# Performance work log

Hardware: AMD Instinct MI355X
Metric: run time of the kernel (lower is better)

The kernel has to match this reference:

```python
import jax, jax.numpy as jnp
import numpy as np

B, S, D = 2, 2048, 2048
H, G = 32, 8            # n_head, n_kv_groups
DH = D // H             # 64
HG = H // G             # heads per group = 4


def setup_inputs() -> dict:
    key = jax.random.key(0)
    ks = jax.random.split(key, 7)
    kv_dim = G * DH
    return {
        "q": jax.random.normal(ks[0], (B, S, D), jnp.float32),
        "k": jax.random.normal(ks[1], (B, S, D), jnp.float32),
        "v": jax.random.normal(ks[2], (B, S, D), jnp.float32),
        "mask": jnp.tril(jnp.ones((S, S), jnp.bool_)),  # causal
        "w_q": jax.random.normal(ks[3], (D, D), jnp.float32) * 0.02,
        "w_k": jax.random.normal(ks[4], (kv_dim, D), jnp.float32) * 0.02,
        "w_v": jax.random.normal(ks[5], (kv_dim, D), jnp.float32) * 0.02,
        "w_out": jax.random.normal(ks[6], (D, D), jnp.float32) * 0.02,
    }


def reference(q, k, v, mask, w_q, w_k, w_v, w_out):
    scale = 1.0 / np.sqrt(DH).astype(np.float32)
    # projections (F.linear: x @ W.T)
    qp = (q @ w_q.T).reshape(B, S, G, HG, DH)   # [b s g h d]
    kp = (k @ w_k.T).reshape(B, S, G, DH)       # [b t g d]
    vp = (v @ w_v.T).reshape(B, S, G, DH)
    # grouped attention scores [b g h s t]
    scores = jnp.einsum('bsghd,btgd->bghst', qp, kp) * scale
    scores = jnp.where(mask[None, None, None], scores, jnp.float32(-jnp.inf))
    attn = jax.nn.softmax(scores, axis=-1)
    out = jnp.einsum('bghst,btgd->bsghd', attn, vp).reshape(B, S, D)
    return out @ w_out.T
```

## Files before the change

kernel.cpp:

```cpp
#include <hip/hip_runtime.h>
#include <hip/hip_bf16.h>
#include <stdint.h>

#define B_SZ 2
#define S_LEN 2048
#define D_MODEL 2048
#define NH 32
#define NG 8
#define HGRP 4
#define DHEAD 64
#define KV_DIM 512
#define M_TOK 4096
#define KVB 64
#define QBLK 256
#define N_ITEMS2 768

typedef __attribute__((ext_vector_type(8))) short bf16x8;
typedef __attribute__((ext_vector_type(4))) float f32x4;
typedef __attribute__((ext_vector_type(16))) float f32x16;

__device__ inline unsigned short f2bf(float x) {
    uint32_t u = __builtin_bit_cast(uint32_t, x);
    uint32_t r = (u + 0x7fffu + ((u >> 16) & 1u)) >> 16;
    return (unsigned short)r;
}

__device__ inline uint32_t cvtpk(float lo, float hi) {
    uint32_t r;
    asm("v_cvt_pk_bf16_f32 %0, %1, %2" : "=v"(r) : "v"(lo), "v"(hi));
    return r;
}

__device__ inline void plswap(uint32_t& a, uint32_t& b) {
    asm volatile("v_permlane32_swap_b32 %0, %1" : "+v"(a), "+v"(b));
}

__device__ inline float bf2f(unsigned short u) {
    uint32_t x = ((uint32_t)u) << 16;
    return __builtin_bit_cast(float, x);
}

__device__ inline void async_copy16(const void* g, void* l) {
    __builtin_amdgcn_global_load_lds(
        (const __attribute__((address_space(1))) void*)g,
        (__attribute__((address_space(3))) void*)l,
        16, 0, 0);
}

__device__ inline void gbar() {
    asm volatile("" ::: "memory");
    __builtin_amdgcn_s_barrier();
    asm volatile("" ::: "memory");
}
__device__ inline void lgkm0() {
    asm volatile("s_waitcnt lgkmcnt(0)" ::: "memory");
    __builtin_amdgcn_sched_barrier(0);
}

__global__ __launch_bounds__(256) void cvt_all(const float* __restrict__ q,
                                               const float* __restrict__ k,
                                               const float* __restrict__ v,
                                               const float* __restrict__ wq,
                                               const float* __restrict__ wk,
                                               const float* __restrict__ wv,
                                               const float* __restrict__ wo,
                                               unsigned short* __restrict__ qb,
                                               unsigned short* __restrict__ kb,
                                               unsigned short* __restrict__ vb,
                                               unsigned short* __restrict__ wqb,
                                               unsigned short* __restrict__ wkvb,
                                               unsigned short* __restrict__ wob,
                                               unsigned int* __restrict__ cnt) {
    const int i = blockIdx.x * 256 + threadIdx.x;
    if (i == 0) *cnt = 0u;
    const float* src; unsigned short* dst; int j;
    if (i < 1048576)      { src = q;  dst = qb;  j = i; }
    else if (i < 2097152) { src = k;  dst = kb;  j = i - 1048576; }
    else if (i < 3145728) { src = v;  dst = vb;  j = i - 2097152; }
    else if (i < 3670016) { src = wq; dst = wqb; j = i - 3145728; }
    else if (i < 3801088) { src = wk; dst = wkvb; j = i - 3670016; }
    else if (i < 3932160) { src = wv; dst = wkvb + (size_t)KV_DIM * D_MODEL; j = i - 3801088; }
    else                  { src = wo; dst = wob; j = i - 3932160; }
    const float4* p = reinterpret_cast<const float4*>(src) + (size_t)j * 2;
    float4 a = p[0], b = p[1];
    union { unsigned short u[8]; uint4 v4; } r;
    r.u[0] = f2bf(a.x); r.u[1] = f2bf(a.y); r.u[2] = f2bf(a.z); r.u[3] = f2bf(a.w);
    r.u[4] = f2bf(b.x); r.u[5] = f2bf(b.y); r.u[6] = f2bf(b.z); r.u[7] = f2bf(b.w);
    reinterpret_cast<uint4*>(dst)[j] = r.v4;
}

#define SCALE_Q 0.1803368867f
#define GK 2048

template<int WHICH>
__global__ __launch_bounds__(512, 2) void gemm8(const unsigned short* __restrict__ Aq,
                                                const unsigned short* __restrict__ Ak,
                                                const unsigned short* __restrict__ Av,
                                                const unsigned short* __restrict__ Bq,
                                                const unsigned short* __restrict__ Bkv,
                                                unsigned short* __restrict__ out_q,
                                                unsigned short* __restrict__ out_k,
                                                unsigned short* __restrict__ out_v,
                                                float* __restrict__ out_f) {
    __shared__ __align__(16) char lds[131072];

    const int tid = threadIdx.x;
    const int lane = tid & 63;
    const int w = tid >> 6;
    const int wm = w >> 2, wn = w & 3;
    const int l15 = lane & 15, l4 = lane >> 4;

    const int nblk = (WHICH == 0) ? 192 : 128;
    int bid = blockIdx.x;
    bid = (bid & 7) * (nblk >> 3) + (bid >> 3);
    const int mb = bid & 15, nb = bid >> 4;
    const int m0 = mb * 256;

    const unsigned short* Ap;
    const unsigned short* Bp;
    int mode = 0, n0q = 0;
    if (WHICH == 1) {
        Ap = Aq; Bp = Bq + (size_t)(nb * 256) * GK; n0q = nb * 256;
    } else if (nb < 8) {
        Ap = Aq; Bp = Bq + (size_t)(nb * 256) * GK; mode = 0; n0q = nb * 256;
    } else if (nb < 10) {
        Ap = Ak; Bp = Bkv + (size_t)((nb - 8) * 256) * GK; mode = 1; n0q = (nb - 8) * 256;
    } else {
        Ap = Av; Bp = Bkv + (size_t)((nb - 10) * 256 + 512) * GK; mode = 2; n0q = (nb - 10) * 256;
    }

    const int srow = tid >> 3;
    const int gcol = (((tid & 7) * 16) ^ ((srow & 7) << 4)) >> 1;
    char* const myl = lds + tid * 16;

    auto stageA = [&](int tile, int half) {
        char* dst = myl + (tile & 1) * 32768 + half * 16384;
        const unsigned short* src = Ap + (size_t)(m0 + half * 128 + srow) * GK + tile * 64 + gcol;
        async_copy16(src, dst);
        async_copy16(src + (size_t)64 * GK, dst + 8192);
    };
    auto stageB = [&](int tile, int half) {
        char* dst = myl + 65536 + (tile & 1) * 32768 + half * 16384;
        const unsigned short* src = Bp + (size_t)(half * 128 + srow) * GK + tile * 64 + gcol;
        async_copy16(src, dst);
        async_copy16(src + (size_t)64 * GK, dst + 8192);
    };

    bf16x8 af[4][2], bf[4][2];
    auto loadA = [&](int buf, int mhalf) {
        const char* base = lds + buf * 32768;
#pragma unroll
        for (int mi = 0; mi < 4; ++mi) {
            const int r = wm * 128 + mhalf * 64 + mi * 16 + l15;
#pragma unroll
            for (int ks = 0; ks < 2; ++ks)
                af[mi][ks] = *reinterpret_cast<const bf16x8*>(
                    base + r * 128 + ((ks * 64 + l4 * 16) ^ ((r & 7) << 4)));
        }
    };
    auto loadB = [&](int buf, int nhalf) {
        const char* base = lds + 65536 + buf * 32768;
#pragma unroll
        for (int ni2 = 0; ni2 < 2; ++ni2) {
            const int ni = nhalf * 2 + ni2;
            const int r = wn * 64 + ni * 16 + l15;
#pragma unroll
            for (int ks = 0; ks < 2; ++ks)
                bf[ni][ks] = *reinterpret_cast<const bf16x8*>(
                    base + r * 128 + ((ks * 64 + l4 * 16) ^ ((r & 7) << 4)));
        }
    };

    f32x4 acc[8][4] = {};
    auto mfma16 = [&](int mq, int nq) {
        __builtin_amdgcn_s_setprio(1);
#pragma unroll
        for (int mi = 0; mi < 4; ++mi)
#pragma unroll
            for (int ni2 = 0; ni2 < 2; ++ni2)
#pragma unroll
                for (int ks = 0; ks < 2; ++ks)
                    acc[mq * 4 + mi][nq * 2 + ni2] = __builtin_amdgcn_mfma_f32_16x16x32_bf16(
                        af[mi][ks], bf[nq * 2 + ni2][ks], acc[mq * 4 + mi][nq * 2 + ni2], 0, 0, 0);
        __builtin_amdgcn_s_setprio(0);
    };

    stageA(0, 0); stageA(0, 1); stageB(0, 0); stageB(0, 1); stageB(1, 0); stageB(1, 1);
    asm volatile("s_waitcnt vmcnt(4)" ::: "memory");
    gbar();

    for (int i = 0; i < 16; ++i) {
        const int u = 2 * i;
        const bool nl = (i < 15);
        loadA(0, 0); loadB(0, 0); stageA(u + 1, 0);
        gbar(); lgkm0(); mfma16(0, 0); gbar();
        loadB(0, 1); stageA(u + 1, 1);
        gbar(); lgkm0(); mfma16(0, 1); gbar();
        loadA(0, 1); if (nl) stageB(u + 2, 0);
        gbar(); lgkm0(); mfma16(1, 0); gbar();
        if (nl) stageB(u + 2, 1);
        gbar(); mfma16(1, 1);
        if (nl) asm volatile("s_waitcnt vmcnt(4)" ::: "memory");
        else    asm volatile("s_waitcnt vmcnt(0)" ::: "memory");
        gbar();
        loadA(1, 0); loadB(1, 0); if (nl) stageA(u + 2, 0);
        gbar(); lgkm0(); mfma16(0, 0); gbar();
        loadB(1, 1); if (nl) stageA(u + 2, 1);
        gbar(); lgkm0(); mfma16(0, 1); gbar();
        loadA(1, 1); if (nl) stageB(u + 3, 0);
        gbar(); lgkm0(); mfma16(1, 0); gbar();
        if (nl) stageB(u + 3, 1);
        gbar(); mfma16(1, 1);
        if (nl) asm volatile("s_waitcnt vmcnt(4)" ::: "memory");
        gbar();
    }

    if (WHICH == 1) {
#pragma unroll
        for (int mi = 0; mi < 8; ++mi) {
            const int row = m0 + wm * 128 + mi * 16 + l4 * 4;
#pragma unroll
            for (int ni = 0; ni < 4; ++ni) {
                const int col = n0q + wn * 64 + ni * 16 + l15;
#pragma unroll
                for (int r = 0; r < 4; ++r)
                    out_f[(size_t)(row + r) * D_MODEL + col] = acc[mi][ni][r];
            }
        }
    } else if (mode == 0) {
#pragma unroll
        for (int mi = 0; mi < 8; ++mi) {
            const int row = m0 + wm * 128 + mi * 16 + l4 * 4;
#pragma unroll
            for (int ni = 0; ni < 4; ++ni) {
                const int col = n0q + wn * 64 + ni * 16 + l15;
#pragma unroll
                for (int r = 0; r < 4; ++r)
                    out_q[(size_t)(row + r) * D_MODEL + col] = f2bf(acc[mi][ni][r] * SCALE_Q);
            }
        }
    } else if (mode == 1) {
#pragma unroll
        for (int mi = 0; mi < 8; ++mi) {
            const int row = m0 + wm * 128 + mi * 16 + l4 * 4;
#pragma unroll
            for (int ni = 0; ni < 4; ++ni) {
                const int col = n0q + wn * 64 + ni * 16 + l15;
#pragma unroll
                for (int r = 0; r < 4; ++r)
                    out_k[(size_t)(row + r) * KV_DIM + col] = f2bf(acc[mi][ni][r]);
            }
        }
    } else {
        const int bb = m0 >> 11;
#pragma unroll
        for (int mi = 0; mi < 8; ++mi) {
            const int tok = (m0 & 2047) + wm * 128 + mi * 16 + l4 * 4;
#pragma unroll
            for (int ni = 0; ni < 4; ++ni) {
                const int c = n0q + wn * 64 + ni * 16 + l15;
                const int g = c >> 6, dh = c & 63;
                uint2 pk;
                pk.x = cvtpk(acc[mi][ni][0], acc[mi][ni][1]);
                pk.y = cvtpk(acc[mi][ni][2], acc[mi][ni][3]);
                *reinterpret_cast<uint2*>(out_v + (size_t)((bb * NG + g) * DHEAD + dh) * S_LEN + tok) = pk;
            }
        }
    }
}

__constant__ unsigned char cls2_qi[12]   = {7,7,3,6,6,5,5,2,4,4,1,0};
__constant__ unsigned char cls2_half[12] = {0,1,0,0,1,0,1,0,0,1,0,0};

__global__ __launch_bounds__(512, 4) void attn3_kernel(const unsigned short* __restrict__ qp,
                                                       const unsigned short* __restrict__ kp,
                                                       const unsigned short* __restrict__ vpT,
                                                       unsigned short* __restrict__ attn_out,
                                                       unsigned int* __restrict__ counter,
                                                       unsigned short* __restrict__ partO,
                                                       float* __restrict__ ml) {
    __shared__ __align__(16) unsigned short Ks[2][KVB * 64];
    __shared__ __align__(16) unsigned short Vs[2][KVB * 64];
    __shared__ int s_item;

    const int tid = threadIdx.x;
    const int lane = tid & 63;
    const int w = tid >> 6;
    const int l31 = lane & 31, hi = lane >> 5;
    const int sr = tid >> 3, sc = tid & 7;
    const int sgcol = (((sc * 16) ^ ((sr & 7) << 4)) >> 1);
    char* const kdst0 = (char*)Ks[0] + tid * 16;
    char* const kdst1 = (char*)Ks[1] + tid * 16;
    char* const vdst0 = (char*)Vs[0] + tid * 16;
    char* const vdst1 = (char*)Vs[1] + tid * 16;

    for (;;) {
        if (tid == 0) s_item = (int)atomicAdd(counter, 1u);
        __syncthreads();
        const int item = s_item;
        if (item >= N_ITEMS2) break;
        const int slot = item >> 6;
        const int bh = item & 63;
        const int qi = cls2_qi[slot];
        const int half = cls2_half[slot];
        const bool split = qi >= 4;
        const int b = bh >> 5, head = bh & 31, g = head >> 2;
        const int s0 = qi * QBLK;
        const int m = s0 + w * 32 + l31;
        const int mmaxw = s0 + w * 32 + 31;

        int j0, j1;
        if (split) { j0 = half * 2 * (qi + 1); j1 = j0 + 2 * (qi + 1); }
        else       { j0 = 0;                   j1 = 4 * (qi + 1); }

        bf16x8 qf[4];
        {
            const unsigned short* qrow = qp + (size_t)(b * S_LEN + m) * D_MODEL + head * DHEAD + hi * 8;
#pragma unroll
            for (int k = 0; k < 4; ++k)
                qf[k] = *reinterpret_cast<const bf16x8*>(qrow + k * 16);
        }

        const unsigned short* kbase = kp + (size_t)(b * S_LEN + sr) * KV_DIM + g * DHEAD + sgcol;
        const unsigned short* vbase = vpT + (size_t)((b * NG + g) * DHEAD + sr) * S_LEN + sgcol;

        float mrun = -1e30f, lrun = 0.f;
        f32x16 o0 = {}, o1 = {};

        async_copy16(kbase + (size_t)j0 * KVB * KV_DIM, kdst0);
        async_copy16(vbase + j0 * KVB, vdst0);
        asm volatile("s_waitcnt vmcnt(0)" ::: "memory");
        gbar();

        for (int j = j0; j < j1; ++j) {
            const int cur = (j - j0) & 1;
            const int t0 = j * KVB;
            if (j + 1 < j1) {
                async_copy16(kbase + (size_t)(j + 1) * KVB * KV_DIM, cur ? kdst0 : kdst1);
                async_copy16(vbase + (j + 1) * KVB, cur ? vdst0 : vdst1);
            }

            const bool tt0 = (t0 <= mmaxw);
            const bool tt1 = (t0 + 32 <= mmaxw);
            if (tt0) {
                const char* Kb = (const char*)Ks[cur];
                const char* Vb = (const char*)Vs[cur];
                const int rswz0 = (l31 & 7) << 4;

                f32x16 s0v = {}, s1v = {};
#pragma unroll
                for (int k = 0; k < 4; ++k) {
                    const int coff = k * 32 + hi * 16;
                    const bf16x8 kf0 = *reinterpret_cast<const bf16x8*>(
                        Kb + l31 * 128 + (coff ^ rswz0));
                    s0v = __builtin_amdgcn_mfma_f32_32x32x16_bf16(kf0, qf[k], s0v, 0, 0, 0);
                    if (tt1) {
                        const bf16x8 kf1 = *reinterpret_cast<const bf16x8*>(
                            Kb + (32 + l31) * 128 + (coff ^ rswz0));
                        s1v = __builtin_amdgcn_mfma_f32_32x32x16_bf16(kf1, qf[k], s1v, 0, 0, 0);
                    }
                }

                const bool msk = (t0 + KVB - 1) > (s0 + w * 32);
                float rmax = -1e30f;
#pragma unroll
                for (int r = 0; r < 16; ++r) {
                    const int tloc = (r & 3) + 8 * (r >> 2) + 4 * hi;
                    float v = s0v[r];
                    if (msk && (t0 + tloc > m)) v = -1e30f;
                    s0v[r] = v;
                    rmax = fmaxf(rmax, v);
                }
                if (tt1) {
#pragma unroll
                    for (int r = 0; r < 16; ++r) {
                        const int tloc = 32 + (r & 3) + 8 * (r >> 2) + 4 * hi;
                        float v = s1v[r];
                        if (msk && (t0 + tloc > m)) v = -1e30f;
                        s1v[r] = v;
                        rmax = fmaxf(rmax, v);
                    }
                }
                rmax = fmaxf(rmax, __shfl_xor(rmax, 32, 64));
                if (!__all(rmax <= mrun + 8.0f)) {
                    const float mnew = fmaxf(mrun, rmax);
                    const float corr = __builtin_amdgcn_exp2f(mrun - mnew);
                    lrun *= corr;
#pragma unroll
                    for (int r = 0; r < 16; ++r) { o0[r] *= corr; o1[r] *= corr; }
                    mrun = mnew;
                }
                float rs = 0.f;
#pragma unroll
                for (int r = 0; r < 16; ++r) {
                    const float p = __builtin_amdgcn_exp2f(s0v[r] - mrun);
                    s0v[r] = p;
                    rs += p;
                }
                if (tt1) {
#pragma unroll
                    for (int r = 0; r < 16; ++r) {
                        const float p = __builtin_amdgcn_exp2f(s1v[r] - mrun);
                        s1v[r] = p;
                        rs += p;
                    }
                }
                rs += __shfl_xor(rs, 32, 64);
                lrun += rs;

#pragma unroll
                for (int c = 0; c < 4; ++c) {
                    if (c >= 2 && !tt1) break;
                    const f32x16& sv = (c >> 1) ? s1v : s0v;
                    const int h8 = (c & 1) * 8;
                    uint32_t a0 = cvtpk(sv[h8 + 0], sv[h8 + 1]);
                    uint32_t a1 = cvtpk(sv[h8 + 2], sv[h8 + 3]);
                    uint32_t b0 = cvtpk(sv[h8 + 4], sv[h8 + 5]);
                    uint32_t b1 = cvtpk(sv[h8 + 6], sv[h8 + 7]);
                    plswap(a0, b0); plswap(a1, b1);
                    union { uint32_t w4[4]; bf16x8 v; } pf;
                    pf.w4[0] = a0; pf.w4[1] = a1; pf.w4[2] = b0; pf.w4[3] = b1;
                    const int coff = c * 32 + hi * 16;
                    const bf16x8 vf0 = *reinterpret_cast<const bf16x8*>(
                        Vb + l31 * 128 + (coff ^ rswz0));
                    o0 = __builtin_amdgcn_mfma_f32_32x32x16_bf16(vf0, pf.v, o0, 0, 0, 0);
                    const bf16x8 vf1 = *reinterpret_cast<const bf16x8*>(
                        Vb + (32 + l31) * 128 + (coff ^ rswz0));
                    o1 = __builtin_amdgcn_mfma_f32_32x32x16_bf16(vf1, pf.v, o1, 0, 0, 0);
                }
            }
            asm volatile("s_waitcnt vmcnt(0)" ::: "memory");
            gbar();
        }

        if (split) {
            const int pb = ((bh << 2) + (qi - 4)) * 2 + half;
            const int mrow = w * 32 + l31;
            if (hi == 0) {
                ml[pb * 512 + mrow] = mrun;
                ml[pb * 512 + 256 + mrow] = lrun;
            }
            unsigned short* dst = partO + (size_t)pb * 16384 + mrow * 64 + hi * 4;
#pragma unroll
            for (int qd = 0; qd < 4; ++qd) {
                uint2 pk0, pk1;
                pk0.x = cvtpk(o0[4 * qd + 0], o0[4 * qd + 1]);
                pk0.y = cvtpk(o0[4 * qd + 2], o0[4 * qd + 3]);
                pk1.x = cvtpk(o1[4 * qd + 0], o1[4 * qd + 1]);
                pk1.y = cvtpk(o1[4 * qd + 2], o1[4 * qd + 3]);
                *reinterpret_cast<uint2*>(dst + 8 * qd) = pk0;
                *reinterpret_cast<uint2*>(dst + 32 + 8 * qd) = pk1;
            }
        } else {
            const float inv = 1.0f / lrun;
            unsigned short* dst = attn_out + (size_t)(b * S_LEN + m) * D_MODEL + head * DHEAD + hi * 4;
#pragma unroll
            for (int qd = 0; qd < 4; ++qd) {
                uint2 pk0, pk1;
                pk0.x = cvtpk(o0[4 * qd + 0] * inv, o0[4 * qd + 1] * inv);
                pk0.y = cvtpk(o0[4 * qd + 2] * inv, o0[4 * qd + 3] * inv);
                pk1.x = cvtpk(o1[4 * qd + 0] * inv, o1[4 * qd + 1] * inv);
                pk1.y = cvtpk(o1[4 * qd + 2] * inv, o1[4 * qd + 3] * inv);
                *reinterpret_cast<uint2*>(dst + 8 * qd) = pk0;
                *reinterpret_cast<uint2*>(dst + 32 + 8 * qd) = pk1;
            }
        }
    }
}

__global__ __launch_bounds__(512) void merge2_kernel(const unsigned short* __restrict__ partO,
                                                     const float* __restrict__ ml,
                                                     unsigned short* __restrict__ attn_out) {
    const int blk = blockIdx.x;
    const int bh = blk >> 2;
    const int qi = (blk & 3) + 4;
    const int b = bh >> 5, head = bh & 31;
    const int s0 = qi * QBLK;
    const int tid = threadIdx.x;
    const int row = tid >> 1, dh0 = (tid & 1) * 32;
    const int pb0 = blk * 2, pb1 = pb0 + 1;

    const float m0 = ml[pb0 * 512 + row], l0 = ml[pb0 * 512 + 256 + row];
    const float m1 = ml[pb1 * 512 + row], l1 = ml[pb1 * 512 + 256 + row];
    const float M = fmaxf(m0, m1);
    float w0 = __builtin_amdgcn_exp2f(m0 - M);
    float w1 = __builtin_amdgcn_exp2f(m1 - M);
    const float inv = 1.0f / (l0 * w0 + l1 * w1);
    w0 *= inv; w1 *= inv;

    const uint4* p0 = reinterpret_cast<const uint4*>(partO + (size_t)pb0 * 16384 + row * 64 + dh0);
    const uint4* p1 = reinterpret_cast<const uint4*>(partO + (size_t)pb1 * 16384 + row * 64 + dh0);
    unsigned short* dst = attn_out + (size_t)(b * S_LEN + s0 + row) * D_MODEL + head * DHEAD + dh0;
#pragma unroll
    for (int c = 0; c < 4; ++c) {
        union { unsigned short u[8]; uint4 v; } ua, ub, uo;
        ua.v = p0[c]; ub.v = p1[c];
#pragma unroll
        for (int e = 0; e < 8; e += 2) {
            float x0 = bf2f(ua.u[e]) * w0 + bf2f(ub.u[e]) * w1;
            float x1 = bf2f(ua.u[e + 1]) * w0 + bf2f(ub.u[e + 1]) * w1;
            reinterpret_cast<uint32_t*>(uo.u)[e >> 1] = cvtpk(x0, x1);
        }
        reinterpret_cast<uint4*>(dst)[c] = uo.v;
    }
}

extern "C" void kernel_launch(void* const* d_in, const int* in_sizes, int n_in,
                              void* d_out, int out_size, void* d_ws, size_t ws_size,
                              hipStream_t stream) {
    const float* q     = (const float*)d_in[0];
    const float* k     = (const float*)d_in[1];
    const float* v     = (const float*)d_in[2];
    const float* w_q   = (const float*)d_in[4];
    const float* w_k   = (const float*)d_in[5];
    const float* w_v   = (const float*)d_in[6];
    const float* w_out = (const float*)d_in[7];

    char* ws = (char*)d_ws;
    size_t off = 0;
    auto alloc = [&](size_t n) { char* p = ws + off; off += (n + 255) & ~(size_t)255; return p; };
    unsigned short* qb   = (unsigned short*)alloc((size_t)M_TOK * D_MODEL * 2);
    unsigned short* kb   = (unsigned short*)alloc((size_t)M_TOK * D_MODEL * 2);
    unsigned short* vb   = (unsigned short*)alloc((size_t)M_TOK * D_MODEL * 2);
    unsigned short* wqb  = (unsigned short*)alloc((size_t)D_MODEL * D_MODEL * 2);
    unsigned short* wkvb = (unsigned short*)alloc((size_t)2 * KV_DIM * D_MODEL * 2);
    unsigned short* wob  = (unsigned short*)alloc((size_t)D_MODEL * D_MODEL * 2);
    unsigned short* qpb  = (unsigned short*)alloc((size_t)M_TOK * D_MODEL * 2);
    unsigned short* kpb  = (unsigned short*)alloc((size_t)M_TOK * KV_DIM * 2);
    unsigned short* vtb  = (unsigned short*)alloc((size_t)M_TOK * KV_DIM * 2);
    unsigned short* aob  = (unsigned short*)alloc((size_t)M_TOK * D_MODEL * 2);
    float*          mlb  = (float*)alloc((size_t)512 * 512 * 4);
    unsigned int*   cnt  = (unsigned int*)alloc(256);

    cvt_all<<<dim3(17408), dim3(256), 0, stream>>>(q, k, v, w_q, w_k, w_v, w_out,
                                                   qb, kb, vb, wqb, wkvb, wob, cnt);

    gemm8<0><<<dim3(192), dim3(512), 0, stream>>>(qb, kb, vb, wqb, wkvb, qpb, kpb, vtb, nullptr);

    attn3_kernel<<<dim3(512), dim3(512), 0, stream>>>(qpb, kpb, vtb, aob, cnt, qb, mlb);
    merge2_kernel<<<dim3(256), dim3(512), 0, stream>>>(qb, mlb, aob);

    gemm8<1><<<dim3(128), dim3(512), 0, stream>>>(aob, nullptr, nullptr, wob, nullptr,
                                                  nullptr, nullptr, nullptr, (float*)d_out);
}
```

Measured before the change: 212.3 us.

## Split output projection into smaller-tile GEMM and hoist causal mask branch

```diff
diff --git a/kernel.cpp b/kernel.cpp
--- a/kernel.cpp
+++ b/kernel.cpp
@@ -92,16 +92,14 @@
 #define SCALE_Q 0.1803368867f
 #define GK 2048
 
-template<int WHICH>
-__global__ __launch_bounds__(512, 2) void gemm8(const unsigned short* __restrict__ Aq,
-                                                const unsigned short* __restrict__ Ak,
-                                                const unsigned short* __restrict__ Av,
-                                                const unsigned short* __restrict__ Bq,
-                                                const unsigned short* __restrict__ Bkv,
-                                                unsigned short* __restrict__ out_q,
-                                                unsigned short* __restrict__ out_k,
-                                                unsigned short* __restrict__ out_v,
-                                                float* __restrict__ out_f) {
+__global__ __launch_bounds__(512, 2) void gemm8p(const unsigned short* __restrict__ Aq,
+                                                 const unsigned short* __restrict__ Ak,
+                                                 const unsigned short* __restrict__ Av,
+                                                 const unsigned short* __restrict__ Bq,
+                                                 const unsigned short* __restrict__ Bkv,
+                                                 unsigned short* __restrict__ out_q,
+                                                 unsigned short* __restrict__ out_k,
+                                                 unsigned short* __restrict__ out_v) {
     __shared__ __align__(16) char lds[131072];
 
     const int tid = threadIdx.x;
@@ -110,18 +108,15 @@
     const int wm = w >> 2, wn = w & 3;
     const int l15 = lane & 15, l4 = lane >> 4;
 
-    const int nblk = (WHICH == 0) ? 192 : 128;
     int bid = blockIdx.x;
-    bid = (bid & 7) * (nblk >> 3) + (bid >> 3);
+    bid = (bid & 7) * 24 + (bid >> 3);
     const int mb = bid & 15, nb = bid >> 4;
     const int m0 = mb * 256;
 
     const unsigned short* Ap;
     const unsigned short* Bp;
     int mode = 0, n0q = 0;
-    if (WHICH == 1) {
-        Ap = Aq; Bp = Bq + (size_t)(nb * 256) * GK; n0q = nb * 256;
-    } else if (nb < 8) {
+    if (nb < 8) {
         Ap = Aq; Bp = Bq + (size_t)(nb * 256) * GK; mode = 0; n0q = nb * 256;
     } else if (nb < 10) {
         Ap = Ak; Bp = Bkv + (size_t)((nb - 8) * 256) * GK; mode = 1; n0q = (nb - 8) * 256;
@@ -215,19 +210,7 @@
         gbar();
     }
 
-    if (WHICH == 1) {
-#pragma unroll
-        for (int mi = 0; mi < 8; ++mi) {
-            const int row = m0 + wm * 128 + mi * 16 + l4 * 4;
-#pragma unroll
-            for (int ni = 0; ni < 4; ++ni) {
-                const int col = n0q + wn * 64 + ni * 16 + l15;
-#pragma unroll
-                for (int r = 0; r < 4; ++r)
-                    out_f[(size_t)(row + r) * D_MODEL + col] = acc[mi][ni][r];
-            }
-        }
-    } else if (mode == 0) {
+    if (mode == 0) {
 #pragma unroll
         for (int mi = 0; mi < 8; ++mi) {
             const int row = m0 + wm * 128 + mi * 16 + l4 * 4;
@@ -265,6 +248,120 @@
                 pk.y = cvtpk(acc[mi][ni][2], acc[mi][ni][3]);
                 *reinterpret_cast<uint2*>(out_v + (size_t)((bb * NG + g) * DHEAD + dh) * S_LEN + tok) = pk;
             }
+        }
+    }
+}
+
+__global__ __launch_bounds__(512, 1) void gemm8o(const unsigned short* __restrict__ A,
+                                                 const unsigned short* __restrict__ B,
+                                                 float* __restrict__ C) {
+    __shared__ __align__(16) char lds[98304];
+
+    const int tid = threadIdx.x;
+    const int lane = tid & 63;
+    const int w = tid >> 6;
+    const int wm = w >> 1, wn = w & 1;
+    const int l15 = lane & 15, l4 = lane >> 4;
+
+    int bid = blockIdx.x;
+    bid = (bid & 7) * 32 + (bid >> 3);
+    const int mb = bid & 15, nb = bid >> 4;
+    const int m0 = mb * 256, n0 = nb * 128;
+    const unsigned short* Bp = B + (size_t)n0 * GK;
+
+    const int srow = tid >> 3;
+    const int gcol = (((tid & 7) * 16) ^ ((srow & 7) << 4)) >> 1;
+
+    auto stageA = [&](int tile, int half) {
+        char* dst = lds + (tile & 1) * 32768 + half * 16384 + tid * 16;
+        const unsigned short* src = A + (size_t)(m0 + half * 128 + srow) * GK + tile * 64 + gcol;
+        async_copy16(src, dst);
+        async_copy16(src + (size_t)64 * GK, dst + 8192);
+    };
+    auto stageB = [&](int tile, int half) {
+        char* dst = lds + 65536 + (tile & 1) * 16384 + half * 8192 + tid * 16;
+        const unsigned short* src = Bp + (size_t)(half * 64 + srow) * GK + tile * 64 + gcol;
+        async_copy16(src, dst);
+    };
+
+    bf16x8 af[2][2], bf[4][2];
+    auto loadA2 = [&](int buf, int mhalf) {
+        const char* base = lds + buf * 32768;
+#pragma unroll
+        for (int mi = 0; mi < 2; ++mi) {
+            const int r = wm * 64 + mhalf * 32 + mi * 16 + l15;
+#pragma unroll
+            for (int ks = 0; ks < 2; ++ks)
+                af[mi][ks] = *reinterpret_cast<const bf16x8*>(
+                    base + r * 128 + ((ks * 64 + l4 * 16) ^ ((r & 7) << 4)));
+        }
+    };
+    auto loadB2 = [&](int buf, int nhalf) {
+        const char* base = lds + 65536 + buf * 16384;
+#pragma unroll
+        for (int ni2 = 0; ni2 < 2; ++ni2) {
+            const int ni = nhalf * 2 + ni2;
+            const int r = wn * 64 + ni * 16 + l15;
+#pragma unroll
+            for (int ks = 0; ks < 2; ++ks)
+                bf[ni][ks] = *reinterpret_cast<const bf16x8*>(
+                    base + r * 128 + ((ks * 64 + l4 * 16) ^ ((r & 7) << 4)));
+        }
+    };
+
+    f32x4 acc[4][4] = {};
+    auto mfma8 = [&](int mq, int nq) {
+        __builtin_amdgcn_s_setprio(1);
+#pragma unroll
+        for (int mi = 0; mi < 2; ++mi)
+#pragma unroll
+            for (int ni2 = 0; ni2 < 2; ++ni2)
+#pragma unroll
+                for (int ks = 0; ks < 2; ++ks)
+                    acc[mq * 2 + mi][nq * 2 + ni2] = __builtin_amdgcn_mfma_f32_16x16x32_bf16(
+                        af[mi][ks], bf[nq * 2 + ni2][ks], acc[mq * 2 + mi][nq * 2 + ni2], 0, 0, 0);
+        __builtin_amdgcn_s_setprio(0);
+    };
+
+    stageA(0, 0); stageA(0, 1); stageB(0, 0); stageB(0, 1); stageB(1, 0); stageB(1, 1);
+    asm volatile("s_waitcnt vmcnt(2)" ::: "memory");
+    gbar();
+
+    for (int i = 0; i < 16; ++i) {
+        const int u = 2 * i;
+        const bool nl = (i < 15);
+        loadA2(0, 0); loadB2(0, 0); stageA(u + 1, 0);
+        gbar(); lgkm0(); mfma8(0, 0); gbar();
+        loadB2(0, 1); stageA(u + 1, 1);
+        gbar(); lgkm0(); mfma8(0, 1); gbar();
+        loadA2(0, 1); if (nl) stageB(u + 2, 0);
+        gbar(); lgkm0(); mfma8(1, 0); gbar();
+        if (nl) stageB(u + 2, 1);
+        gbar(); mfma8(1, 1);
+        if (nl) asm volatile("s_waitcnt vmcnt(2)" ::: "memory");
+        else    asm volatile("s_waitcnt vmcnt(0)" ::: "memory");
+        gbar();
+        loadA2(1, 0); loadB2(1, 0); if (nl) stageA(u + 2, 0);
+        gbar(); lgkm0(); mfma8(0, 0); gbar();
+        loadB2(1, 1); if (nl) stageA(u + 2, 1);
+        gbar(); lgkm0(); mfma8(0, 1); gbar();
+        loadA2(1, 1); if (nl) stageB(u + 3, 0);
+        gbar(); lgkm0(); mfma8(1, 0); gbar();
+        if (nl) stageB(u + 3, 1);
+        gbar(); mfma8(1, 1);
+        if (nl) asm volatile("s_waitcnt vmcnt(2)" ::: "memory");
+        gbar();
+    }
+
+#pragma unroll
+    for (int mi = 0; mi < 4; ++mi) {
+        const int row = m0 + wm * 64 + mi * 16 + l4 * 4;
+#pragma unroll
+        for (int ni = 0; ni < 4; ++ni) {
+            const int col = n0 + wn * 64 + ni * 16 + l15;
+#pragma unroll
+            for (int r = 0; r < 4; ++r)
+                C[(size_t)(row + r) * D_MODEL + col] = acc[mi][ni][r];
         }
     }
 }
@@ -363,22 +460,33 @@
 
                 const bool msk = (t0 + KVB - 1) > (s0 + w * 32);
                 float rmax = -1e30f;
-#pragma unroll
-                for (int r = 0; r < 16; ++r) {
-                    const int tloc = (r & 3) + 8 * (r >> 2) + 4 * hi;
-                    float v = s0v[r];
-                    if (msk && (t0 + tloc > m)) v = -1e30f;
-                    s0v[r] = v;
-                    rmax = fmaxf(rmax, v);
-                }
-                if (tt1) {
+                if (msk) {
 #pragma unroll
                     for (int r = 0; r < 16; ++r) {
-                        const int tloc = 32 + (r & 3) + 8 * (r >> 2) + 4 * hi;
-                        float v = s1v[r];
-                        if (msk && (t0 + tloc > m)) v = -1e30f;
-                        s1v[r] = v;
+                        const int tloc = (r & 3) + 8 * (r >> 2) + 4 * hi;
+                        float v = s0v[r];
+                        if (t0 + tloc > m) v = -1e30f;
+                        s0v[r] = v;
                         rmax = fmaxf(rmax, v);
+                    }
+                    if (tt1) {
+#pragma unroll
+                        for (int r = 0; r < 16; ++r) {
+                            const int tloc = 32 + (r & 3) + 8 * (r >> 2) + 4 * hi;
+                            float v = s1v[r];
+                            if (t0 + tloc > m) v = -1e30f;
+                            s1v[r] = v;
+                            rmax = fmaxf(rmax, v);
+                        }
+                    }
+                } else {
+#pragma unroll
+                    for (int r = 0; r < 16; ++r)
+                        rmax = fmaxf(rmax, s0v[r]);
+                    if (tt1) {
+#pragma unroll
+                        for (int r = 0; r < 16; ++r)
+                            rmax = fmaxf(rmax, s1v[r]);
                     }
                 }
                 rmax = fmaxf(rmax, __shfl_xor(rmax, 32, 64));
@@ -535,11 +643,10 @@
     cvt_all<<<dim3(17408), dim3(256), 0, stream>>>(q, k, v, w_q, w_k, w_v, w_out,
                                                    qb, kb, vb, wqb, wkvb, wob, cnt);
 
-    gemm8<0><<<dim3(192), dim3(512), 0, stream>>>(qb, kb, vb, wqb, wkvb, qpb, kpb, vtb, nullptr);
-
-    attn3_kernel<<<dim3(512), dim3(512), 0, stream>>>(qpb, kpb, vtb, aob, cnt, qb, mlb);
+    gemm8p<<<dim3(192), dim3(512), 0, stream>>>(qb, kb, vb, wqb, wkvb, qpb, kpb, vtb);
+
+    attn3_kernel<<<dim3(768), dim3(512), 0, stream>>>(qpb, kpb, vtb, aob, cnt, qb, mlb);
     merge2_kernel<<<dim3(256), dim3(512), 0, stream>>>(qb, mlb, aob);
 
-    gemm8<1><<<dim3(128), dim3(512), 0, stream>>>(aob, nullptr, nullptr, wob, nullptr,
-                                                  nullptr, nullptr, nullptr, (float*)d_out);
-}
+    gemm8o<<<dim3(256), dim3(512), 0, stream>>>(aob, wob, (float*)d_out);
+}
```

Result: faster. 189.3 us (-10.8%).
